# Optimization experiments

Hardware: AMD Instinct MI355X
Metric: run time of the kernel (lower is better)

Reference implementation:

```python
import jax, jax.numpy as jnp
import numpy as np

NEG_INF = -1e10
SLOPE = 0.01  # LeakyReLU default negative slope

def _lrelu(x):
    return jnp.where(x >= 0, x, SLOPE * x)

def setup_inputs() -> dict:
    key = jax.random.key(0)
    ks = jax.random.split(key, 12)
    B, L, D = 64, 512, 512
    s = 1.0 / np.sqrt(D)
    s2 = 1.0 / np.sqrt(2 * D)
    return {
        "r1": jax.random.normal(ks[0], (B, L, D), jnp.float32),
        "r2": jax.random.normal(ks[1], (B, L, D), jnp.float32),
        "mask1": jax.random.randint(ks[2], (B, L, 1), 0, 2, jnp.int32),
        "mask2": jax.random.randint(ks[3], (B, L, 1), 0, 2, jnp.int32),
        # mlp params (shared for r1 and r2, as in the torch module)
        "W1": jax.random.uniform(ks[4], (D, D), jnp.float32, -s, s),
        "b1": jnp.zeros((D,), jnp.float32),
        "W2": jax.random.uniform(ks[5], (D, D), jnp.float32, -s, s),
        "b2": jnp.zeros((D,), jnp.float32),
        # compare params
        "Wc1": jax.random.uniform(ks[6], (2 * D, D), jnp.float32, -s2, s2),
        "bc1": jnp.zeros((D,), jnp.float32),
        "Wc2": jax.random.uniform(ks[7], (D, D), jnp.float32, -s, s),
        "bc2": jnp.zeros((D,), jnp.float32),
    }

def reference(r1, r2, mask1, mask2, W1, b1, W2, b2, Wc1, bc1, Wc2, bc2):
    # dropout is inference-mode identity
    def mlp(x):
        return _lrelu(_lrelu(x @ W1 + b1) @ W2 + b2)

    def compare(x):
        return _lrelu(_lrelu(x @ Wc1 + bc1) @ Wc2 + bc2)

    m1 = mask1.astype(jnp.float32)  # [B,L1,1]
    m2 = mask2.astype(jnp.float32)  # [B,L2,1]
    r1m = mlp(r1) * m1
    r2m = mlp(r2) * m2

    # pairwise mask: >0 iff both tokens valid (magnitude from the D-dim matmul is irrelevant)
    mpos = m1 * jnp.swapaxes(m2, 1, 2)            # [B,L1,L2] in {0,1}
    mask_inf = jnp.where(mpos > 0, 0.0, NEG_INF)  # additive mask

    o = jnp.einsum('bik,bjk->bij', r1m, r2m) + mask_inf  # [B,L1,L2]
    o1 = jax.nn.softmax(o, axis=2) * mpos
    o2 = jax.nn.softmax(o, axis=1) * mpos

    r1_c = jnp.einsum('bij,bjd->bid', o1, r2m)  # [B,L1,D]
    r2_c = jnp.einsum('bij,bid->bjd', o2, r1m)  # [B,L2,D]

    r1_cmp = compare(jnp.concatenate([r1m, r1_c], axis=-1)) * m1
    r2_cmp = compare(jnp.concatenate([r2m, r2_c], axis=-1)) * m2
    return (r1_cmp, r2_cmp)
```

## Files before the change

### kernel.cpp

```cpp
#include <hip/hip_runtime.h>

#define LRELU_SLOPE 0.01f
#define NEG_BIG -1e10f

typedef unsigned short ushort_t;
typedef __bf16 bf16x8 __attribute__((ext_vector_type(8)));
typedef float f32x4 __attribute__((ext_vector_type(4)));

static __device__ __forceinline__ float lrelu_f(float x) {
    return x >= 0.0f ? x : LRELU_SLOPE * x;
}

static __device__ __forceinline__ ushort_t f2bf(float f) {
    unsigned int u = __float_as_uint(f);
    u += 0x7fffu + ((u >> 16) & 1u);
    return (ushort_t)(u >> 16);
}

static __device__ __forceinline__ void gld_lds16(const ushort_t* g, ushort_t* l) {
    __builtin_amdgcn_global_load_lds((const __attribute__((address_space(1))) void*)g,
                                     (__attribute__((address_space(3))) void*)l,
                                     16, 0, 0);
}

template<bool BIAS, bool LRELU, bool RM, bool PM, bool BF16OUT, bool TWOUT>
__global__ __launch_bounds__(256)
void gemm_nt(const ushort_t* __restrict__ A0, const ushort_t* __restrict__ A1,
             int Ksplit, int lda0, int lda1,
             const ushort_t* __restrict__ B, int ldb,
             const float* __restrict__ bias,
             const int* __restrict__ rm1, const int* __restrict__ rm2,
             void* __restrict__ C, int ldc,
             ushort_t* __restrict__ CT, int Mhalf,
             int M, int N, int K,
             long sA, long sB, long sC)
{
    __shared__ ushort_t As[128 * 32];
    __shared__ ushort_t Bs[128 * 32];

    const unsigned nbx = gridDim.x, nby = gridDim.y;
    unsigned lin = blockIdx.x + nbx * (blockIdx.y + nby * blockIdx.z);
    const unsigned nwg = nbx * nby * gridDim.z;
    if ((nwg & 7u) == 0u)
        lin = (lin & 7u) * (nwg >> 3) + (lin >> 3);
    const unsigned bxs = lin % nbx;
    const unsigned t1  = lin / nbx;
    const unsigned bys = t1 % nby;
    const unsigned bzs = t1 / nby;

    const int bz   = (int)bzs;
    const int tid  = threadIdx.x;
    const int w    = tid >> 6;
    const int lane = tid & 63;
    const int wm   = w & 1;
    const int wn   = w >> 1;
    const int row0 = (int)bys * 128;
    const int col0 = (int)bxs * 128;

    const ushort_t* Ab0 = A0 + (long)bz * sA;
    const ushort_t* Ab1 = A1 + (long)bz * sA;
    const ushort_t* Bb  = B  + (long)bz * sB;

    const int sRow = w * 32 + (lane >> 2);
    const int sOff = (((lane & 3) ^ ((lane >> 3) & 3)) * 8);
    ushort_t* ldsA0 = &As[w * 1024];
    ushort_t* ldsA1 = &As[w * 1024 + 512];
    ushort_t* ldsB0 = &Bs[w * 1024];
    ushort_t* ldsB1 = &Bs[w * 1024 + 512];

    const int lr = lane & 15, q = lane >> 4;
    const int aBase = (wm * 64 + lr) * 32 + (q ^ ((lr >> 1) & 3)) * 8;
    const int bBase = (wn * 64 + lr) * 32 + (q ^ ((lr >> 1) & 3)) * 8;

    f32x4 acc[4][4] = {};

    for (int k0 = 0; k0 < K; k0 += 32) {
        const ushort_t* Ap; int kk, ldaP;
        if (k0 < Ksplit) { Ap = Ab0; kk = k0;          ldaP = lda0; }
        else             { Ap = Ab1; kk = k0 - Ksplit; ldaP = lda1; }

        gld_lds16(Ap + (size_t)(row0 + sRow) * ldaP + kk + sOff, ldsA0);
        gld_lds16(Ap + (size_t)(row0 + sRow + 16) * ldaP + kk + sOff, ldsA1);
        gld_lds16(Bb + (size_t)(col0 + sRow) * ldb + k0 + sOff, ldsB0);
        gld_lds16(Bb + (size_t)(col0 + sRow + 16) * ldb + k0 + sOff, ldsB1);

        __syncthreads();

        bf16x8 af[4], bf[4];
        #pragma unroll
        for (int i = 0; i < 4; ++i)
            af[i] = *reinterpret_cast<const bf16x8*>(&As[aBase + i * 16 * 32]);
        #pragma unroll
        for (int j = 0; j < 4; ++j)
            bf[j] = *reinterpret_cast<const bf16x8*>(&Bs[bBase + j * 16 * 32]);
        #pragma unroll
        for (int i = 0; i < 4; ++i)
            #pragma unroll
            for (int j = 0; j < 4; ++j)
                acc[i][j] = __builtin_amdgcn_mfma_f32_16x16x32_bf16(af[i], bf[j], acc[i][j], 0, 0, 0);

        __syncthreads();
    }

    float biasv[4];
    int mj[4];
    #pragma unroll
    for (int j = 0; j < 4; ++j) {
        const int c = col0 + wn * 64 + j * 16 + lr;
        if (BIAS) biasv[j] = bias[c];
        if (PM)   mj[j] = rm2[(long)bz * N + c];
    }
    float* Cf = (float*)C + (long)bz * sC;
    ushort_t* Ch = (ushort_t*)C + (long)bz * sC;

    #pragma unroll
    for (int i = 0; i < 4; ++i) {
        const int rg0 = row0 + wm * 64 + i * 16 + q * 4;
        int mi4[4];
        if (RM || PM) {
            #pragma unroll
            for (int r = 0; r < 4; ++r) {
                const int row = rg0 + r;
                if (PM)      mi4[r] = rm1[(long)bz * M + row];
                else         mi4[r] = (row < Mhalf) ? rm1[row] : rm2[row - Mhalf];
            }
        }
        #pragma unroll
        for (int j = 0; j < 4; ++j) {
            const int c = col0 + wn * 64 + j * 16 + lr;
            ushort_t tp[4];
            #pragma unroll
            for (int r = 0; r < 4; ++r) {
                const int row = rg0 + r;
                float v = acc[i][j][r];
                if (BIAS) v += biasv[j];
                if (LRELU) v = lrelu_f(v);
                if (RM) v *= (float)mi4[r];
                if (PM) { if (!(mi4[r] && mj[j])) v += NEG_BIG; }
                const size_t a = (size_t)row * ldc + c;
                if (BF16OUT) Ch[a] = f2bf(v); else Cf[a] = v;
                if (TWOUT) tp[r] = f2bf(v);
            }
            if (TWOUT) {
                const size_t ta = ((size_t)(((rg0 >> 9) + 64) & 127)) * 262144
                                + (size_t)c * 512 + (rg0 & 511);
                *reinterpret_cast<uint2*>(CT + ta) = *reinterpret_cast<uint2*>(tp);
            }
        }
    }
}

__global__ __launch_bounds__(256)
void cvt2_f32_bf16(const float* __restrict__ a, const float* __restrict__ b,
                   ushort_t* __restrict__ oa, ushort_t* __restrict__ ob)
{
    const float* in = blockIdx.y ? b : a;
    ushort_t* out = blockIdx.y ? ob : oa;
    const long i = ((long)blockIdx.x * 256 + threadIdx.x) * 4;
    const float4 v = *reinterpret_cast<const float4*>(in + i);
    ushort_t o[4] = { f2bf(v.x), f2bf(v.y), f2bf(v.z), f2bf(v.w) };
    *reinterpret_cast<uint2*>(out + i) = *reinterpret_cast<uint2*>(o);
}

__global__ __launch_bounds__(256)
void transpose_cvt4(const float* __restrict__ W1, const float* __restrict__ W2,
                    const float* __restrict__ Wc1, const float* __restrict__ Wc2,
                    ushort_t* __restrict__ W1t, ushort_t* __restrict__ W2t,
                    ushort_t* __restrict__ Wc1t, ushort_t* __restrict__ Wc2t)
{
    __shared__ float t[32][33];
    const int z = blockIdx.z;
    const float* in = (z == 0) ? W1 : (z == 1) ? W2 : (z == 2) ? Wc1 : Wc2;
    ushort_t* out   = (z == 0) ? W1t : (z == 1) ? W2t : (z == 2) ? Wc1t : Wc2t;
    const int R = (z == 2) ? 1024 : 512;
    const int C = 512;
    const int c0 = blockIdx.x * 32, r0 = blockIdx.y * 32;
    if (r0 >= R) return;
    const int tx = threadIdx.x & 31, ty = threadIdx.x >> 5;
    #pragma unroll
    for (int p = 0; p < 4; ++p)
        t[ty + p * 8][tx] = in[(size_t)(r0 + ty + p * 8) * C + c0 + tx];
    __syncthreads();
    #pragma unroll
    for (int p = 0; p < 4; ++p)
        out[(size_t)(c0 + ty + p * 8) * R + r0 + tx] = f2bf(t[tx][ty + p * 8]);
}

__global__ __launch_bounds__(256)
void row_stats(const float* __restrict__ o, float* __restrict__ rmax,
               float* __restrict__ rsinv, int L)
{
    const int row  = blockIdx.x * 4 + (threadIdx.x >> 6);
    const int lane = threadIdx.x & 63;
    const float* p = o + (long)row * L;
    float m = -3.0e38f;
    for (int j = lane; j < L; j += 64) m = fmaxf(m, p[j]);
    #pragma unroll
    for (int off = 32; off > 0; off >>= 1) m = fmaxf(m, __shfl_xor(m, off));
    float s = 0.0f;
    for (int j = lane; j < L; j += 64) s += __expf(p[j] - m);
    #pragma unroll
    for (int off = 32; off > 0; off >>= 1) s += __shfl_xor(s, off);
    if (lane == 0) { rmax[row] = m; rsinv[row] = 1.0f / s; }
}

__global__ __launch_bounds__(256)
void col_part(const float* __restrict__ o, float* __restrict__ pm,
              float* __restrict__ ps, int L)
{
    const int b  = blockIdx.z;
    const int rc = blockIdx.y;
    const int j  = blockIdx.x * 256 + threadIdx.x;
    const float* p = o + (long)b * L * L + (long)rc * 64 * L + j;
    float m = -3.0e38f, s = 0.0f;
    #pragma unroll 4
    for (int i = 0; i < 64; ++i) {
        const float x = p[(long)i * L];
        const float mn = fmaxf(m, x);
        s = s * __expf(m - mn) + __expf(x - mn);
        m = mn;
    }
    const long idx = ((long)b * 8 + rc) * L + j;
    pm[idx] = m;
    ps[idx] = s;
}

__global__ __launch_bounds__(256)
void col_combine(const float* __restrict__ pm, const float* __restrict__ ps,
                 float* __restrict__ cmax, float* __restrict__ csinv, int L)
{
    const int b = blockIdx.y;
    const int j = blockIdx.x * 256 + threadIdx.x;
    float mk[8], sk[8];
    #pragma unroll
    for (int k = 0; k < 8; ++k) {
        mk[k] = pm[((long)b * 8 + k) * L + j];
        sk[k] = ps[((long)b * 8 + k) * L + j];
    }
    float m = -3.0e38f;
    #pragma unroll
    for (int k = 0; k < 8; ++k) m = fmaxf(m, mk[k]);
    float s = 0.0f;
    #pragma unroll
    for (int k = 0; k < 8; ++k) s += sk[k] * __expf(mk[k] - m);
    cmax[b * L + j]  = m;
    csinv[b * L + j] = 1.0f / s;
}

__global__ __launch_bounds__(256)
void softmax_apply(const float* __restrict__ o,
                   ushort_t* __restrict__ o1, ushort_t* __restrict__ o2T,
                   const float* __restrict__ rmax, const float* __restrict__ rsinv,
                   const float* __restrict__ cmax, const float* __restrict__ csinv,
                   const int* __restrict__ m1, const int* __restrict__ m2)
{
    __shared__ ushort_t t[32][33];
    const int b = blockIdx.z;
    const long bo = (long)b * 512 * 512;
    const int j0 = blockIdx.x * 32, i0 = blockIdx.y * 32;
    const int tx = threadIdx.x & 31, ty = threadIdx.x >> 5;
    const int col = b * 512 + j0 + tx;
    const int mjv = m2[col];
    const float cm = cmax[col], cs = csinv[col];
    #pragma unroll
    for (int p = 0; p < 4; ++p) {
        const int i = i0 + ty + p * 8;
        const int row = b * 512 + i;
        const float x = o[bo + (long)i * 512 + j0 + tx];
        const float mp = (m1[row] != 0 && mjv != 0) ? 1.0f : 0.0f;
        o1[bo + (long)i * 512 + j0 + tx] = f2bf(__expf(x - rmax[row]) * rsinv[row] * mp);
        t[ty + p * 8][tx] = f2bf(__expf(x - cm) * cs * mp);
    }
    __syncthreads();
    #pragma unroll
    for (int p = 0; p < 4; ++p)
        o2T[bo + (long)(j0 + ty + p * 8) * 512 + i0 + tx] = t[tx][ty + p * 8];
}

extern "C" void kernel_launch(void* const* d_in, const int* in_sizes, int n_in,
                              void* d_out, int out_size, void* d_ws, size_t ws_size,
                              hipStream_t stream)
{
    const float* r1  = (const float*)d_in[0];
    const float* r2  = (const float*)d_in[1];
    const int*   m1  = (const int*)d_in[2];
    const int*   m2  = (const int*)d_in[3];
    const float* W1  = (const float*)d_in[4];
    const float* b1v = (const float*)d_in[5];
    const float* W2  = (const float*)d_in[6];
    const float* b2v = (const float*)d_in[7];
    const float* Wc1 = (const float*)d_in[8];
    const float* bc1 = (const float*)d_in[9];
    const float* Wc2 = (const float*)d_in[10];
    const float* bc2 = (const float*)d_in[11];
    float* out = (float*)d_out;

    constexpr int  Bn = 64, L = 512, D = 512;
    constexpr long CE = (long)Bn * L * D;
    constexpr long S  = (long)L * L;
    constexpr int  NR = Bn * L;

    ushort_t* O    = (ushort_t*)d_out;
    ushort_t* r1b  = O;
    ushort_t* r2b  = O + CE;
    ushort_t* TT   = O;
    ushort_t* o1b  = O + 2 * CE;
    ushort_t* o2Tb = O + 3 * CE;

    char* wsb = (char*)d_ws;
    ushort_t* hb   = (ushort_t*)wsb;
    float*    obuf = (float*)wsb;
    ushort_t* r1c  = (ushort_t*)wsb;
    ushort_t* hc   = (ushort_t*)(wsb + 4 * CE);
    ushort_t* r1mb = (ushort_t*)(wsb + 8 * CE);
    ushort_t* r2mb = (ushort_t*)(wsb + 10 * CE);
    ushort_t* W1t  = (ushort_t*)(wsb + 12 * CE);
    ushort_t* W2t  = W1t + 512 * 512;
    ushort_t* Wc1t = W2t + 512 * 512;
    ushort_t* Wc2t = Wc1t + 512 * 1024;
    float* rmaxv = (float*)(Wc2t + 512 * 512);
    float* rsinv = rmaxv + NR;
    float* cmaxv = rsinv + NR;
    float* csinv = cmaxv + NR;
    float* pmbuf = csinv + NR;
    float* psbuf = pmbuf + 8 * L * Bn;

    const dim3 blk(256);
    const dim3 gD2(D / 128, 2 * NR / 128, 1);
    const dim3 gB(L / 128, L / 128, Bn);
    const dim3 gB2(L / 128, L / 128, 2 * Bn);

    cvt2_f32_bf16<<<dim3(CE / 1024, 2), blk, 0, stream>>>(r1, r2, r1b, r2b);
    transpose_cvt4<<<dim3(16, 32, 4), blk, 0, stream>>>(
        W1, W2, Wc1, Wc2, W1t, W2t, Wc1t, Wc2t);

    gemm_nt<true,true,false,false,true,false><<<gD2, blk, 0, stream>>>(
        r1b, r1b, D, D, D, W1t, D, b1v, nullptr, nullptr, hb, D,
        nullptr, 0, 2 * NR, D, D, 0, 0, 0);
    gemm_nt<true,true,true,false,true,true><<<gD2, blk, 0, stream>>>(
        hb, hb, D, D, D, W2t, D, b2v, m1, m2, r1mb, D,
        TT, NR, 2 * NR, D, D, 0, 0, 0);
    gemm_nt<false,false,false,true,false,false><<<gB, blk, 0, stream>>>(
        r1mb, r1mb, D, D, D, r2mb, D, nullptr, m1, m2, obuf, L,
        nullptr, 0, L, L, D, S, S, S);
    row_stats<<<dim3(NR / 4), blk, 0, stream>>>(obuf, rmaxv, rsinv, L);
    col_part<<<dim3(L / 256, 8, Bn), blk, 0, stream>>>(obuf, pmbuf, psbuf, L);
    col_combine<<<dim3(L / 256, Bn), blk, 0, stream>>>(pmbuf, psbuf, cmaxv, csinv, L);
    softmax_apply<<<dim3(16, 16, Bn), blk, 0, stream>>>(
        obuf, o1b, o2Tb, rmaxv, rsinv, cmaxv, csinv, m1, m2);
    gemm_nt<false,false,false,false,true,false><<<gB2, blk, 0, stream>>>(
        o1b, o1b, L, L, L, TT, L, nullptr, nullptr, nullptr, r1c, D,
        nullptr, 0, L, D, L, S, S, S);
    gemm_nt<true,true,false,false,true,false><<<gD2, blk, 0, stream>>>(
        r1mb, r1c, D, D, D, Wc1t, 2 * D, bc1, nullptr, nullptr, hc, D,
        nullptr, 0, 2 * NR, D, 2 * D, 0, 0, 0);
    gemm_nt<true,true,true,false,false,false><<<gD2, blk, 0, stream>>>(
        hc, hc, D, D, D, Wc2t, D, bc2, m1, m2, out, D,
        nullptr, NR, 2 * NR, D, D, 0, 0, 0);
}
```

Before: 684.8 us.

## Double-buffer LDS tiles in GEMM to overlap global loads with MFMA

Measured after the change: 674.8 us. About the same (-1.5%).

```diff
diff --git a/kernel.cpp b/kernel.cpp
--- a/kernel.cpp
+++ b/kernel.cpp
@@ -35,8 +35,8 @@
              int M, int N, int K,
              long sA, long sB, long sC)
 {
-    __shared__ ushort_t As[128 * 32];
-    __shared__ ushort_t Bs[128 * 32];
+    __shared__ ushort_t As[2][128 * 32];
+    __shared__ ushort_t Bs[2][128 * 32];
 
     const unsigned nbx = gridDim.x, nby = gridDim.y;
     unsigned lin = blockIdx.x + nbx * (blockIdx.y + nby * blockIdx.z);
@@ -63,10 +63,6 @@
 
     const int sRow = w * 32 + (lane >> 2);
     const int sOff = (((lane & 3) ^ ((lane >> 3) & 3)) * 8);
-    ushort_t* ldsA0 = &As[w * 1024];
-    ushort_t* ldsA1 = &As[w * 1024 + 512];
-    ushort_t* ldsB0 = &Bs[w * 1024];
-    ushort_t* ldsB1 = &Bs[w * 1024 + 512];
 
     const int lr = lane & 15, q = lane >> 4;
     const int aBase = (wm * 64 + lr) * 32 + (q ^ ((lr >> 1) & 3)) * 8;
@@ -74,32 +70,48 @@
 
     f32x4 acc[4][4] = {};
 
-    for (int k0 = 0; k0 < K; k0 += 32) {
+    auto stage = [&](int k0g, ushort_t* Ad, ushort_t* Bd) {
         const ushort_t* Ap; int kk, ldaP;
-        if (k0 < Ksplit) { Ap = Ab0; kk = k0;          ldaP = lda0; }
-        else             { Ap = Ab1; kk = k0 - Ksplit; ldaP = lda1; }
-
-        gld_lds16(Ap + (size_t)(row0 + sRow) * ldaP + kk + sOff, ldsA0);
-        gld_lds16(Ap + (size_t)(row0 + sRow + 16) * ldaP + kk + sOff, ldsA1);
-        gld_lds16(Bb + (size_t)(col0 + sRow) * ldb + k0 + sOff, ldsB0);
-        gld_lds16(Bb + (size_t)(col0 + sRow + 16) * ldb + k0 + sOff, ldsB1);
-
-        __syncthreads();
+        if (k0g < Ksplit) { Ap = Ab0; kk = k0g;          ldaP = lda0; }
+        else              { Ap = Ab1; kk = k0g - Ksplit; ldaP = lda1; }
+        gld_lds16(Ap + (size_t)(row0 + sRow) * ldaP + kk + sOff, Ad + w * 1024);
+        gld_lds16(Ap + (size_t)(row0 + sRow + 16) * ldaP + kk + sOff, Ad + w * 1024 + 512);
+        gld_lds16(Bb + (size_t)(col0 + sRow) * ldb + k0g + sOff, Bd + w * 1024);
+        gld_lds16(Bb + (size_t)(col0 + sRow + 16) * ldb + k0g + sOff, Bd + w * 1024 + 512);
+    };
+
+    const int NT = K >> 5;
+    stage(0, As[0], Bs[0]);
+
+    for (int t = 0; t < NT; ++t) {
+        ushort_t* Ac = As[t & 1];
+        ushort_t* Bc = Bs[t & 1];
+
+        if (t + 1 < NT) {
+            stage((t + 1) << 5, As[(t + 1) & 1], Bs[(t + 1) & 1]);
+            asm volatile("s_waitcnt vmcnt(4)" ::: "memory");
+        } else {
+            asm volatile("s_waitcnt vmcnt(0)" ::: "memory");
+        }
+        __builtin_amdgcn_s_barrier();
 
         bf16x8 af[4], bf[4];
         #pragma unroll
         for (int i = 0; i < 4; ++i)
-            af[i] = *reinterpret_cast<const bf16x8*>(&As[aBase + i * 16 * 32]);
+            af[i] = *reinterpret_cast<const bf16x8*>(&Ac[aBase + i * 16 * 32]);
         #pragma unroll
         for (int j = 0; j < 4; ++j)
-            bf[j] = *reinterpret_cast<const bf16x8*>(&Bs[bBase + j * 16 * 32]);
+            bf[j] = *reinterpret_cast<const bf16x8*>(&Bc[bBase + j * 16 * 32]);
         #pragma unroll
         for (int i = 0; i < 4; ++i)
             #pragma unroll
             for (int j = 0; j < 4; ++j)
                 acc[i][j] = __builtin_amdgcn_mfma_f32_16x16x32_bf16(af[i], bf[j], acc[i][j], 0, 0, 0);
 
-        __syncthreads();
+        if (t + 1 < NT) {
+            asm volatile("s_waitcnt lgkmcnt(0)" ::: "memory");
+            __builtin_amdgcn_s_barrier();
+        }
     }
 
     float biasv[4];
```
